# Optimization experiments

Measured on AMD Instinct MI355X. Metric: run time of the kernel, lower is better.

## Reference

```python
import jax, jax.numpy as jnp
import numpy as np

B, ENC, Hh, Ww = 32, 512, 14, 14
ATT, EMB, DEC, VOCAB = 512, 512, 512, 10000
MAXLEN = 64  # decode steps = MAXLEN - 1 = 63


def setup_inputs() -> dict:
    key = jax.random.key(0)
    ks = iter(jax.random.split(key, 40))
    def p(shape, s=0.02):
        return jax.random.normal(next(ks), shape, dtype=jnp.float32) * s
    encoder_out = jax.random.normal(next(ks), (B, ENC, Hh, Ww), dtype=jnp.float32)
    encoded_captions = jax.random.randint(next(ks), (B, MAXLEN), 0, VOCAB)
    lens = jax.random.randint(next(ks), (B,), 2, MAXLEN + 1)
    caption_lengths = jnp.sort(lens)[::-1].at[0].set(MAXLEN)  # sorted desc, max forced
    return {
        'encoder_out': encoder_out,
        'encoded_captions': encoded_captions,
        'caption_lengths': caption_lengths,
        'emb_table': p((VOCAB, EMB)),
        'W_enc_att': p((ENC, ATT)), 'b_enc_att': jnp.zeros((ATT,), jnp.float32),
        'W_dec_att': p((DEC, ATT)), 'b_dec_att': jnp.zeros((ATT,), jnp.float32),
        'W_full_att': p((ATT, 1)), 'b_full_att': jnp.zeros((1,), jnp.float32),
        'W_init_h': p((ENC, DEC)), 'b_init_h': jnp.zeros((DEC,), jnp.float32),
        'W_init_c': p((ENC, DEC)), 'b_init_c': jnp.zeros((DEC,), jnp.float32),
        'W_f_beta': p((DEC, ENC)), 'b_f_beta': jnp.zeros((ENC,), jnp.float32),
        'W_ih': p((EMB + ENC, 4 * DEC)), 'b_ih': jnp.zeros((4 * DEC,), jnp.float32),
        'W_hh': p((DEC, 4 * DEC)), 'b_hh': jnp.zeros((4 * DEC,), jnp.float32),
        'W_fc': p((DEC, VOCAB)), 'b_fc': jnp.zeros((VOCAB,), jnp.float32),
    }


def reference(encoder_out, encoded_captions, caption_lengths, emb_table,
              W_enc_att, b_enc_att, W_dec_att, b_dec_att, W_full_att, b_full_att,
              W_init_h, b_init_h, W_init_c, b_init_c, W_f_beta, b_f_beta,
              W_ih, b_ih, W_hh, b_hh, W_fc, b_fc):
    Bs, C, H, W = encoder_out.shape
    enc = encoder_out.transpose(0, 2, 3, 1).reshape(Bs, H * W, C)   # [B,P,ENC]
    emb = emb_table[encoded_captions]                               # [B,L,EMB]
    mean_enc = enc.mean(axis=1)
    h0 = mean_enc @ W_init_h + b_init_h
    c0 = mean_enc @ W_init_c + b_init_c
    dec_len = caption_lengths - 1                                   # [B]
    T = encoded_captions.shape[1] - 1                               # static 63
    enc_att = enc @ W_enc_att + b_enc_att                           # precomputed [B,P,ATT]
    emb_steps = jnp.swapaxes(emb[:, :T, :], 0, 1)                   # [T,B,EMB]
    ts = jnp.arange(T)

    def step(carry, xs):
        h, c = carry
        e_t, t = xs
        # additive attention: full_att(relu(enc_att(enc) + dec_att(h)))
        dec_a = h @ W_dec_att + b_dec_att                           # [B,ATT]
        score = (jax.nn.relu(enc_att + dec_a[:, None, :]) @ W_full_att)[..., 0] + b_full_att[0]
        alpha = jax.nn.softmax(score, axis=1)                       # [B,P]
        awe = jnp.einsum('bp,bpc->bc', alpha, enc)                  # [B,ENC]
        gate = jax.nn.sigmoid(h @ W_f_beta + b_f_beta)
        x = jnp.concatenate([e_t, gate * awe], axis=1)              # [B,EMB+ENC]
        gates = x @ W_ih + b_ih + h @ W_hh + b_hh                   # torch LSTMCell: i,f,g,o
        i, f, g, o = jnp.split(gates, 4, axis=1)
        c_new = jax.nn.sigmoid(f) * c + jax.nn.sigmoid(i) * jnp.tanh(g)
        h_new = jax.nn.sigmoid(o) * jnp.tanh(c_new)
        mask = (t < dec_len)[:, None]                               # active prefix (sorted lens)
        preds = jnp.where(mask, h_new @ W_fc + b_fc, 0.0)           # dropout in eval = identity
        h = jnp.where(mask, h_new, h)
        c = jnp.where(mask, c_new, c)
        return (h, c), preds

    (_, _), preds = jax.lax.scan(step, (h0, c0), (emb_steps, ts))
    return jnp.swapaxes(preds, 0, 1)                                # [B,T,VOCAB]
```

## Files before the change

### kernel.cpp

```cpp
#include <hip/hip_runtime.h>
#include <cstdint>
#include <cstddef>

typedef _Float16 f16;
typedef _Float16 h2 __attribute__((ext_vector_type(2)));
typedef _Float16 h8 __attribute__((ext_vector_type(8)));
typedef float f4v __attribute__((ext_vector_type(4)));

__device__ __forceinline__ h2 u2h2(unsigned u) { return __builtin_bit_cast(h2, u); }
__device__ __forceinline__ unsigned h22u(h2 v) { return __builtin_bit_cast(unsigned, v); }
__device__ __forceinline__ float2 u2f2(unsigned long long u) { return __builtin_bit_cast(float2, u); }

__device__ __forceinline__ float agent_ld_f(const float* p) {
    return __hip_atomic_load(p, __ATOMIC_RELAXED, __HIP_MEMORY_SCOPE_AGENT);
}
__device__ __forceinline__ void agent_st_f(float* p, float v) {
    __hip_atomic_store(p, v, __ATOMIC_RELAXED, __HIP_MEMORY_SCOPE_AGENT);
}
__device__ __forceinline__ void agent_add_f(float* p, float v) {
    __hip_atomic_fetch_add(p, v, __ATOMIC_RELAXED, __HIP_MEMORY_SCOPE_AGENT);
}
__device__ __forceinline__ unsigned agent_ld_u(const unsigned* p) {
    return __hip_atomic_load(p, __ATOMIC_RELAXED, __HIP_MEMORY_SCOPE_AGENT);
}
__device__ __forceinline__ void agent_st_u(unsigned* p, unsigned v) {
    __hip_atomic_store(p, v, __ATOMIC_RELAXED, __HIP_MEMORY_SCOPE_AGENT);
}
__device__ __forceinline__ unsigned long long agent_ld_u64(const unsigned long long* p) {
    return __hip_atomic_load(p, __ATOMIC_RELAXED, __HIP_MEMORY_SCOPE_AGENT);
}

__device__ __forceinline__ float fdot2(h2 a, h2 b, float c) {
#if __has_builtin(__builtin_amdgcn_fdot2)
    return __builtin_amdgcn_fdot2(a, b, c, false);
#else
    return c + (float)a.x * (float)b.x + (float)a.y * (float)b.y;
#endif
}
__device__ __forceinline__ float sigf(float x) { return 1.0f / (1.0f + expf(-x)); }

__device__ __forceinline__ void gbar32(unsigned* gflags, unsigned epoch, int local) {
    __syncthreads();
    if (threadIdx.x < 64) {
        if (threadIdx.x == 0) {
            asm volatile("s_waitcnt vmcnt(0)" ::: "memory");
            __hip_atomic_store(&gflags[local], epoch, __ATOMIC_RELAXED, __HIP_MEMORY_SCOPE_AGENT);
        }
        const int l = threadIdx.x & 31;
        bool ok;
        do {
            ok = (__hip_atomic_load(&gflags[l], __ATOMIC_RELAXED,
                                    __HIP_MEMORY_SCOPE_AGENT) >= epoch);
            if (!ok) __builtin_amdgcn_s_sleep(1);
        } while (__ballot(ok) != ~0ull);
        asm volatile("" ::: "memory");
    }
    __syncthreads();
}

__global__ void k_prep_w(const float* W_enc, const float* W_dec, const float* W_fb,
                         const float* b_dec, const float* b_fb,
                         const float* b_ih, const float* b_hh,
                         f16* W_encT, f16* Wdf8, float* b_df, float* b_cat) {
    const int S0 = 512 * 512;
    const int S2 = 512 * 1024;
    const int total = S0 + S2 + 1024 + 2048;
    for (int idx = blockIdx.x * 256 + threadIdx.x; idx < total; idx += gridDim.x * 256) {
        int i = idx;
        if (i < S0) { int n = i >> 9, k = i & 511; W_encT[i] = (f16)W_enc[k * 512 + n]; continue; }
        i -= S0;
        if (i < S2) {
            int k8 = i / 8192, r = i % 8192, col = r >> 3, kr = r & 7;
            int k = k8 * 8 + kr;
            float v = (col < 512) ? W_dec[k * 512 + col] : W_fb[k * 512 + (col - 512)];
            Wdf8[i] = (f16)v;
            continue;
        }
        i -= S2;
        if (i < 1024) { b_df[i] = (i < 512) ? b_dec[i] : b_fb[i - 512]; continue; }
        i -= 1024;
        b_cat[i] = b_ih[i] + b_hh[i];
    }
}

__global__ void k_tr_fc(const float* W_fc, f16* W_fcT) {
    __shared__ float tile[64][65];
    int n0 = blockIdx.x * 64;
    int k0 = blockIdx.y * 64;
    int t = threadIdx.x;
#pragma unroll
    for (int i = 0; i < 16; ++i) {
        int lin = t + i * 256;
        int kl = lin >> 6, nl = lin & 63;
        int n = n0 + nl;
        tile[kl][nl] = (n < 10000) ? W_fc[(long)(k0 + kl) * 10000 + n] : 0.0f;
    }
    __syncthreads();
#pragma unroll
    for (int i = 0; i < 2; ++i) {
        int lin = t + i * 256;
        int r = lin >> 3, cv = lin & 7;
        f16 v[8];
#pragma unroll
        for (int kr = 0; kr < 8; ++kr) v[kr] = (f16)tile[cv * 8 + kr][r];
        *(uint4*)&W_fcT[(long)(n0 + r) * 512 + k0 + cv * 8] = *(uint4*)v;
    }
}

__global__ void k_pack_part(const float* W_ih, const float* W_hh, f16* Wpart8) {
    __shared__ float tile[64][65];
    int k0 = blockIdx.x * 64;
    int n0 = blockIdx.y * 64;
    int t = threadIdx.x;
#pragma unroll
    for (int i = 0; i < 16; ++i) {
        int lin = t + i * 256;
        int kl = lin >> 6, nl = lin & 63;
        int k = k0 + kl;
        float v = (k < 512) ? W_ih[(long)k * 2048 + n0 + nl]
                            : W_hh[(long)(k - 512) * 2048 + n0 + nl];
        tile[kl][nl] = v;
    }
    __syncthreads();
#pragma unroll
    for (int i = 0; i < 2; ++i) {
        int lin = t + i * 256;
        int nl = lin & 63, k8l = lin >> 6;
        f16 v[8];
#pragma unroll
        for (int kr = 0; kr < 8; ++kr) v[kr] = (f16)tile[k8l * 8 + kr][nl];
        *(uint4*)&Wpart8[(long)(k0 / 8 + k8l) * 16384 + (long)(n0 + nl) * 8] = *(uint4*)v;
    }
}

__global__ void k_pack_mid(const float* W_ih, f16* Wmid8) {
    __shared__ float tile[64][65];
    int k0 = blockIdx.x * 64;
    int n0 = blockIdx.y * 64;
    int t = threadIdx.x;
#pragma unroll
    for (int i = 0; i < 16; ++i) {
        int lin = t + i * 256;
        int kl = lin >> 6, nl = lin & 63;
        tile[kl][nl] = W_ih[(long)(512 + k0 + kl) * 2048 + n0 + nl];
    }
    __syncthreads();
#pragma unroll
    for (int i = 0; i < 2; ++i) {
        int lin = t + i * 256;
        int nl = lin & 63, k8l = lin >> 6;
        f16 v[8];
#pragma unroll
        for (int kr = 0; kr < 8; ++kr) v[kr] = (f16)tile[k8l * 8 + kr][nl];
        *(uint4*)&Wmid8[(long)(k0 / 8 + k8l) * 16384 + (long)(n0 + nl) * 8] = *(uint4*)v;
    }
}

__global__ void k_prep_enc(const float* enc_out, f16* enc_t, float* mean_enc) {
    __shared__ float tile[64][197];
    int b = blockIdx.x >> 3, cc = blockIdx.x & 7, c0 = cc * 64;
    int t = threadIdx.x;
    const float* src = enc_out + ((long)b * 512 + c0) * 196;
    for (int i = 0; i < 49; ++i) {
        int lin = t + i * 256;
        int cl = lin / 196, p = lin % 196;
        tile[cl][p] = src[cl * 196 + p];
    }
    __syncthreads();
    if (t < 64) {
        float s = 0.f;
        for (int p = 0; p < 196; ++p) s += tile[t][p];
        mean_enc[b * 512 + c0 + t] = s * (1.0f / 196.0f);
    }
    __syncthreads();
    int cl = t & 63, pg = t >> 6;
    for (int i = 0; i < 49; ++i) {
        int p = pg * 49 + i;
        enc_t[((long)(b * 196 + p)) * 512 + c0 + cl] = (f16)tile[cl][p];
    }
}

__global__ void k_h0c0(const float* mean_enc, const float* W_init_h, const float* b_init_h,
                       const float* W_init_c, const float* b_init_c,
                       float* c, f16* h_h, f16* h_all, unsigned* bar) {
    if (blockIdx.x == 64) {
        int t = threadIdx.x;
        for (int i = t; i < 512; i += 256) bar[i] = 0u;
        for (int i = t; i < 32 * 512; i += 256) h_all[(long)2016 * 512 + i] = (f16)0.0f;
        return;
    }
    __shared__ float ms[512];
    int b = blockIdx.x >> 1, which = blockIdx.x & 1;
    const float* W = which ? W_init_c : W_init_h;
    const float* bb = which ? b_init_c : b_init_h;
    int t = threadIdx.x;
    ms[t] = mean_enc[b * 512 + t];
    ms[t + 256] = mean_enc[b * 512 + t + 256];
    __syncthreads();
    for (int jj = 0; jj < 2; ++jj) {
        int j = t + jj * 256;
        float acc = bb[j];
        for (int k = 0; k < 512; ++k) acc += ms[k] * W[k * 512 + j];
        if (which) c[b * 512 + j] = acc;
        else h_h[b * 512 + j] = (f16)acc;
    }
}

__global__ __launch_bounds__(256, 2) void k_encatt(const f16* A, const f16* Bt,
                                                   const float* bias, f16* Cout) {
    __shared__ __align__(16) f16 As[128 * 32];
    __shared__ __align__(16) f16 Bs[128 * 32];
    int m0 = blockIdx.x * 128, n0 = blockIdx.y * 128;
    int t = threadIdx.x, w = t >> 6, lane = t & 63;
    int wm = (w >> 1) * 64, wn = (w & 1) * 64;
    int lm = lane & 15, lq = lane >> 4;
    f4v acc[4][4];
    for (int mi = 0; mi < 4; ++mi)
        for (int ni = 0; ni < 4; ++ni) acc[mi][ni] = (f4v){0.f, 0.f, 0.f, 0.f};
    for (int kb = 0; kb < 512; kb += 32) {
        for (int i = 0; i < 2; ++i) {
            int li = t + i * 256;
            int row = li >> 2, q = li & 3;
            *(uint4*)&As[row * 32 + q * 8] = *(const uint4*)&A[(long)(m0 + row) * 512 + kb + q * 8];
            *(uint4*)&Bs[row * 32 + q * 8] = *(const uint4*)&Bt[(long)(n0 + row) * 512 + kb + q * 8];
        }
        __syncthreads();
        h8 af[4], bf[4];
        for (int i = 0; i < 4; ++i) {
            af[i] = *(const h8*)&As[(wm + i * 16 + lm) * 32 + lq * 8];
            bf[i] = *(const h8*)&Bs[(wn + i * 16 + lm) * 32 + lq * 8];
        }
        for (int mi = 0; mi < 4; ++mi)
            for (int ni = 0; ni < 4; ++ni)
                acc[mi][ni] = __builtin_amdgcn_mfma_f32_16x16x32_f16(af[mi], bf[ni], acc[mi][ni], 0, 0, 0);
        __syncthreads();
    }
    for (int mi = 0; mi < 4; ++mi)
        for (int ni = 0; ni < 4; ++ni)
            for (int r = 0; r < 4; ++r) {
                int row = m0 + wm + mi * 16 + lq * 4 + r;
                int col = n0 + wn + ni * 16 + lm;
                Cout[(long)row * 512 + col] = (f16)(acc[mi][ni][r] + bias[col]);
            }
}

__global__ __launch_bounds__(256, 2) void k_fc(const f16* A, const f16* Bt, const float* bias,
                                               const int* cl, float* out) {
    __shared__ __align__(16) f16 As[128 * 32];
    __shared__ __align__(16) f16 Bs[128 * 32];
    int m0 = blockIdx.x * 128, n0 = blockIdx.y * 128;
    int t = threadIdx.x, w = t >> 6, lane = t & 63;
    int wm = (w >> 1) * 64, wn = (w & 1) * 64;
    int lm = lane & 15, lq = lane >> 4;

    bool myact = false;
    if (t < 128) {
        int row = m0 + t;
        if (row < 2016) {
            int b = row / 63, tt = row - b * 63;
            myact = tt < (cl[b] - 1);
        }
    }
    int anyact = __syncthreads_or((int)myact);
    if (!anyact) {
        for (int i = 0; i < 64; ++i) {
            int idx = t + i * 256;
            int row = m0 + (idx >> 7), col = n0 + (idx & 127);
            if (row < 2016 && col < 10000) out[(long)row * 10000 + col] = 0.0f;
        }
        return;
    }

    f4v acc[4][4];
    for (int mi = 0; mi < 4; ++mi)
        for (int ni = 0; ni < 4; ++ni) acc[mi][ni] = (f4v){0.f, 0.f, 0.f, 0.f};
    for (int kb = 0; kb < 512; kb += 32) {
        for (int i = 0; i < 2; ++i) {
            int li = t + i * 256;
            int row = li >> 2, q = li & 3;
            *(uint4*)&As[row * 32 + q * 8] = *(const uint4*)&A[(long)(m0 + row) * 512 + kb + q * 8];
            *(uint4*)&Bs[row * 32 + q * 8] = *(const uint4*)&Bt[(long)(n0 + row) * 512 + kb + q * 8];
        }
        __syncthreads();
        h8 af[4], bf[4];
        for (int i = 0; i < 4; ++i) {
            af[i] = *(const h8*)&As[(wm + i * 16 + lm) * 32 + lq * 8];
            bf[i] = *(const h8*)&Bs[(wn + i * 16 + lm) * 32 + lq * 8];
        }
        for (int mi = 0; mi < 4; ++mi)
            for (int ni = 0; ni < 4; ++ni)
                acc[mi][ni] = __builtin_amdgcn_mfma_f32_16x16x32_f16(af[mi], bf[ni], acc[mi][ni], 0, 0, 0);
        __syncthreads();
    }
    for (int mi = 0; mi < 4; ++mi)
        for (int ni = 0; ni < 4; ++ni)
            for (int r = 0; r < 4; ++r) {
                int row = m0 + wm + mi * 16 + lq * 4 + r;
                int col = n0 + wn + ni * 16 + lm;
                if (row < 2016 && col < 10000) {
                    int b = row / 63, tt = row - b * 63;
                    bool act = tt < (cl[b] - 1);
                    out[(long)row * 10000 + col] = act ? (acc[mi][ni][r] + bias[col]) : 0.0f;
                }
            }
}

__global__ __launch_bounds__(512, 1) void k_loop(
    const f16* Wdf8, const float* b_df,
    const f16* Wpart8, const f16* Wmid8, const float* b_cat,
    const f16* enc_att_h, const f16* enc_t,
    const float* W_full, const float* emb, const int* caps, const int* cl,
    float* c, f16* h_h, float* da_gp, float* awe2, float* psum2,
    f16* h_all, unsigned* bar) {
    __shared__ __align__(16) unsigned xcat[4 * 512];
    __shared__ float gred[8 * 4 * 64];
    __shared__ float dfred[512];
    __shared__ float gp_loc[4 * 64];
    __shared__ float das2[512];
    __shared__ float es[32];
    __shared__ float ps4[4];
    __shared__ __align__(16) unsigned xms[4 * 256];
    __shared__ float g3[8 * 4 * 64];
    __shared__ float gsm[256];
    __shared__ __align__(16) f16 ea_s[25 * 512];
    __shared__ __align__(16) f16 et_s[512 * 26];

    const int bid = blockIdx.x, t = threadIdx.x;
    const int lane = t & 63, w = t >> 6;
    const int local = bid & 31;
    unsigned* gflags = bar + (bid >> 5) * 32;

    const int bg = bid >> 5, b0 = bg * 4;
    const int cg = bid & 31;
    const int jg = bid & 31;
    const int b2 = b0 + ((bid >> 3) & 3), pg = bid & 7;
    const int nr = (196 - pg * 25) < 25 ? (196 - pg * 25) : 25;

    float4 wfa = *(const float4*)(W_full + lane * 8);
    float4 wfb = *(const float4*)(W_full + lane * 8 + 4);
    const int nc3 = ((t & 63) >> 4) * 512 + jg * 16 + (t & 15);
    float bc_g = 0.f, bdf = 0.f;
    if (t < 256) bc_g = b_cat[nc3];
    if (t < 128) bdf = b_df[cg * 32 + (t & 31)];
    const int myb = b0 + (t >> 3);
    const int mycl = (t < 32) ? cl[myb] : 0;
    const int jp = t & 7;
    const int j0 = jg * 16 + jp * 2;
    const int n1 = (lane >> 4) * 512 + cg * 16 + (lane & 15);
    const int n3 = n1;
    const int dfcol = cg * 32 + (lane & 31);
    const int ksub = lane >> 5, wb2 = w & 3, kh = w >> 2;

    int steps_g;
    {
        int c0v = cl[b0], c1v = cl[b0 + 1], c2v = cl[b0 + 2], c3v = cl[b0 + 3];
        int m01 = c0v > c1v ? c0v : c1v;
        int m23 = c2v > c3v ? c2v : c3v;
        steps_g = (m01 > m23 ? m01 : m23) - 1;
    }

    {
        int r = t >> 6, cv = t & 63;
        for (int base = 0; base < 25; base += 8) {
            int rr = base + r;
            if (rr < nr) {
                const long rowoff = ((long)b2 * 196 + pg * 25 + rr) * 512 + cv * 8;
                uint4 va = *(const uint4*)(enc_att_h + rowoff);
                *(uint4*)&ea_s[rr * 512 + cv * 8] = va;
                uint4 vt = *(const uint4*)(enc_t + rowoff);
                f16 tmp[8]; *(uint4*)tmp = vt;
#pragma unroll
                for (int e = 0; e < 8; ++e) et_s[(cv * 8 + e) * 26 + rr] = tmp[e];
            }
        }
    }

    for (int step = 0; step < steps_g; ++step) {
        {
            if (t < 64) {
                int idx = local * 64 + t;
                agent_st_f(awe2 + (long)(b0 + (idx >> 9)) * 512 + (idx & 511), 0.f);
            }
            if (local == 0 && t < 4) agent_st_f(psum2 + b0 + t, 0.f);
#pragma unroll
            for (int i = 0; i < 2; ++i) {
                int idx = t + i * 512;
                int b = idx >> 8, off = idx & 255;
                int tok = caps[(b0 + b) * 64 + step];
                float2 ev = *(const float2*)(emb + (long)tok * 512 + off * 2);
                h2 pe; pe.x = (f16)ev.x; pe.y = (f16)ev.y;
                xcat[b * 512 + off] = h22u(pe);
                xcat[b * 512 + 256 + off] = agent_ld_u((const unsigned*)h_h + (b0 + b) * 256 + off);
            }
            __syncthreads();
            {
                const f16* wp = Wpart8 + (long)n1 * 8;
                float a0 = 0.f, a1 = 0.f, a2 = 0.f, a3 = 0.f;
                for (int kk = 0; kk < 16; ++kk) {
                    int k8 = w * 16 + kk;
                    uint4 wv = *(const uint4*)(wp + (long)k8 * 16384);
                    uint4 x0 = *(const uint4*)&xcat[0 * 512 + k8 * 4];
                    uint4 x1 = *(const uint4*)&xcat[1 * 512 + k8 * 4];
                    uint4 x2 = *(const uint4*)&xcat[2 * 512 + k8 * 4];
                    uint4 x3 = *(const uint4*)&xcat[3 * 512 + k8 * 4];
                    a0 = fdot2(u2h2(x0.x), u2h2(wv.x), a0);
                    a0 = fdot2(u2h2(x0.y), u2h2(wv.y), a0);
                    a0 = fdot2(u2h2(x0.z), u2h2(wv.z), a0);
                    a0 = fdot2(u2h2(x0.w), u2h2(wv.w), a0);
                    a1 = fdot2(u2h2(x1.x), u2h2(wv.x), a1);
                    a1 = fdot2(u2h2(x1.y), u2h2(wv.y), a1);
                    a1 = fdot2(u2h2(x1.z), u2h2(wv.z), a1);
                    a1 = fdot2(u2h2(x1.w), u2h2(wv.w), a1);
                    a2 = fdot2(u2h2(x2.x), u2h2(wv.x), a2);
                    a2 = fdot2(u2h2(x2.y), u2h2(wv.y), a2);
                    a2 = fdot2(u2h2(x2.z), u2h2(wv.z), a2);
                    a2 = fdot2(u2h2(x2.w), u2h2(wv.w), a2);
                    a3 = fdot2(u2h2(x3.x), u2h2(wv.x), a3);
                    a3 = fdot2(u2h2(x3.y), u2h2(wv.y), a3);
                    a3 = fdot2(u2h2(x3.z), u2h2(wv.z), a3);
                    a3 = fdot2(u2h2(x3.w), u2h2(wv.w), a3);
                }
                gred[(w * 4 + 0) * 64 + lane] = a0;
                gred[(w * 4 + 1) * 64 + lane] = a1;
                gred[(w * 4 + 2) * 64 + lane] = a2;
                gred[(w * 4 + 3) * 64 + lane] = a3;
            }
            {
                const f16* wdf = Wdf8 + (long)dfcol * 8;
                const unsigned* hx = &xcat[wb2 * 512 + 256];
                int kbase = kh * 32 + ksub * 16;
                float a = 0.f;
                for (int kk = 0; kk < 16; ++kk) {
                    int k8 = kbase + kk;
                    uint4 wv = *(const uint4*)(wdf + (long)k8 * 8192);
                    uint4 xv = *(const uint4*)&hx[k8 * 4];
                    a = fdot2(u2h2(xv.x), u2h2(wv.x), a);
                    a = fdot2(u2h2(xv.y), u2h2(wv.y), a);
                    a = fdot2(u2h2(xv.z), u2h2(wv.z), a);
                    a = fdot2(u2h2(xv.w), u2h2(wv.w), a);
                }
                dfred[(wb2 * 32 + (lane & 31)) * 4 + kh * 2 + ksub] = a;
            }
            __syncthreads();
            if (t < 256) {
                int b = t >> 6, col = t & 63;
                float v = bc_g;
#pragma unroll
                for (int ww = 0; ww < 8; ++ww) v += gred[(ww * 4 + b) * 64 + col];
                gp_loc[b * 64 + col] = v;
            }
            if (t < 128) {
                int b = t >> 5, col = t & 31;
                const float* dr = &dfred[(b * 32 + col) * 4];
                float v = dr[0] + dr[1] + dr[2] + dr[3] + bdf;
                agent_st_f(da_gp + (long)(b0 + b) * 1024 + cg * 32 + col, v);
            }
        }
        gbar32(gflags, (unsigned)step * 3u + 1u, local);

        {
            das2[t] = agent_ld_f(da_gp + (long)b2 * 1024 + t);
            __syncthreads();
            float4 dv0 = *(const float4*)&das2[lane * 8];
            float4 dv1 = *(const float4*)&das2[lane * 8 + 4];
#pragma unroll
            for (int i = 0; i < 4; ++i) {
                int r = w + i * 8;
                if (r < nr) {
                    uint4 ev = *(const uint4*)&ea_s[r * 512 + lane * 8];
                    h2 e0 = u2h2(ev.x), e1 = u2h2(ev.y), e2 = u2h2(ev.z), e3 = u2h2(ev.w);
                    float a = 0.f;
                    a += fmaxf((float)e0.x + dv0.x, 0.f) * wfa.x;
                    a += fmaxf((float)e0.y + dv0.y, 0.f) * wfa.y;
                    a += fmaxf((float)e1.x + dv0.z, 0.f) * wfa.z;
                    a += fmaxf((float)e1.y + dv0.w, 0.f) * wfa.w;
                    a += fmaxf((float)e2.x + dv1.x, 0.f) * wfb.x;
                    a += fmaxf((float)e2.y + dv1.y, 0.f) * wfb.y;
                    a += fmaxf((float)e3.x + dv1.z, 0.f) * wfb.z;
                    a += fmaxf((float)e3.y + dv1.w, 0.f) * wfb.w;
                    for (int m = 32; m; m >>= 1) a += __shfl_xor(a, m);
                    if (lane == 0) es[r] = expf(a);
                }
            }
            __syncthreads();
            {
                float acc = 0.f;
                for (int r = 0; r < nr; ++r) acc += es[r] * (float)et_s[t * 26 + r];
                agent_add_f(awe2 + (long)b2 * 512 + t, acc);
                if (t == 0) {
                    float s = 0.f;
                    for (int r = 0; r < nr; ++r) s += es[r];
                    agent_add_f(psum2 + b2, s);
                }
            }
        }
        gbar32(gflags, (unsigned)step * 3u + 2u, local);

        {
            if (t < 4) ps4[t] = 1.0f / agent_ld_f(psum2 + b0 + t);
            __syncthreads();
#pragma unroll
            for (int i = 0; i < 2; ++i) {
                int idx = t + i * 512;
                int bb = idx >> 8, cp = idx & 255;
                float2 aw = u2f2(agent_ld_u64(
                    (const unsigned long long*)awe2 + (long)(b0 + bb) * 256 + cp));
                float inv = ps4[bb];
                float2 fb = u2f2(agent_ld_u64(
                    (const unsigned long long*)da_gp + (long)(b0 + bb) * 512 + 256 + cp));
                h2 pa;
                pa.x = (f16)(sigf(fb.x) * aw.x * inv);
                pa.y = (f16)(sigf(fb.y) * aw.y * inv);
                xms[bb * 256 + cp] = h22u(pa);
            }
            __syncthreads();
            {
                const f16* wp = Wmid8 + (long)n3 * 8;
                float a0 = 0.f, a1 = 0.f, a2 = 0.f, a3 = 0.f;
                for (int kk = 0; kk < 8; ++kk) {
                    int k8 = w * 8 + kk;
                    uint4 wv = *(const uint4*)(wp + (long)k8 * 16384);
                    uint4 x0 = *(const uint4*)&xms[0 * 256 + k8 * 4];
                    uint4 x1 = *(const uint4*)&xms[1 * 256 + k8 * 4];
                    uint4 x2 = *(const uint4*)&xms[2 * 256 + k8 * 4];
                    uint4 x3 = *(const uint4*)&xms[3 * 256 + k8 * 4];
                    a0 = fdot2(u2h2(x0.x), u2h2(wv.x), a0);
                    a0 = fdot2(u2h2(x0.y), u2h2(wv.y), a0);
                    a0 = fdot2(u2h2(x0.z), u2h2(wv.z), a0);
                    a0 = fdot2(u2h2(x0.w), u2h2(wv.w), a0);
                    a1 = fdot2(u2h2(x1.x), u2h2(wv.x), a1);
                    a1 = fdot2(u2h2(x1.y), u2h2(wv.y), a1);
                    a1 = fdot2(u2h2(x1.z), u2h2(wv.z), a1);
                    a1 = fdot2(u2h2(x1.w), u2h2(wv.w), a1);
                    a2 = fdot2(u2h2(x2.x), u2h2(wv.x), a2);
                    a2 = fdot2(u2h2(x2.y), u2h2(wv.y), a2);
                    a2 = fdot2(u2h2(x2.z), u2h2(wv.z), a2);
                    a2 = fdot2(u2h2(x2.w), u2h2(wv.w), a2);
                    a3 = fdot2(u2h2(x3.x), u2h2(wv.x), a3);
                    a3 = fdot2(u2h2(x3.y), u2h2(wv.y), a3);
                    a3 = fdot2(u2h2(x3.z), u2h2(wv.z), a3);
                    a3 = fdot2(u2h2(x3.w), u2h2(wv.w), a3);
                }
                g3[(w * 4 + 0) * 64 + lane] = a0;
                g3[(w * 4 + 1) * 64 + lane] = a1;
                g3[(w * 4 + 2) * 64 + lane] = a2;
                g3[(w * 4 + 3) * 64 + lane] = a3;
            }
            __syncthreads();
            if (t < 256) {
                int b = t >> 6, l2 = t & 63;
                float v = gp_loc[b * 64 + l2];
#pragma unroll
                for (int ww = 0; ww < 8; ++ww) v += g3[(ww * 4 + b) * 64 + l2];
                gsm[b * 64 + l2] = v;
            }
            __syncthreads();
            if (t < 32) {
                int bl = t >> 3;
                int l0 = jp * 2, l1 = jp * 2 + 1;
                float gi0 = gsm[bl * 64 + l0],      gi1 = gsm[bl * 64 + l1];
                float gf0 = gsm[bl * 64 + 16 + l0], gf1 = gsm[bl * 64 + 16 + l1];
                float gg0 = gsm[bl * 64 + 32 + l0], gg1 = gsm[bl * 64 + 32 + l1];
                float go0 = gsm[bl * 64 + 48 + l0], go1 = gsm[bl * 64 + 48 + l1];
                float2 cold = *(float2*)(c + (long)myb * 512 + j0);
                float cn0 = sigf(gf0) * cold.x + sigf(gi0) * tanhf(gg0);
                float hn0 = sigf(go0) * tanhf(cn0);
                float cn1 = sigf(gf1) * cold.y + sigf(gi1) * tanhf(gg1);
                float hn1 = sigf(go1) * tanhf(cn1);
                h2 oldh = u2h2(agent_ld_u((const unsigned*)h_h + myb * 256 + (j0 >> 1)));
                bool act = step < (mycl - 1);
                float hv0, hv1, cv0, cv1;
                if (act) { hv0 = hn0; hv1 = hn1; cv0 = cn0; cv1 = cn1; }
                else { hv0 = (float)oldh.x; hv1 = (float)oldh.y; cv0 = cold.x; cv1 = cold.y; }
                float2 cw; cw.x = cv0; cw.y = cv1;
                *(float2*)(c + (long)myb * 512 + j0) = cw;
                h2 hp; hp.x = (f16)hv0; hp.y = (f16)hv1;
                unsigned pv = h22u(hp);
                agent_st_u((unsigned*)h_h + myb * 256 + (j0 >> 1), pv);
                *((unsigned*)h_all + ((long)myb * 63 + step) * 256 + (j0 >> 1)) = pv;
            }
        }
        gbar32(gflags, (unsigned)step * 3u + 3u, local);
    }
}

extern "C" void kernel_launch(void* const* d_in, const int* in_sizes, int n_in,
                              void* d_out, int out_size, void* d_ws, size_t ws_size,
                              hipStream_t stream) {
    const float* encoder_out = (const float*)d_in[0];
    const int* caps = (const int*)d_in[1];
    const int* cl = (const int*)d_in[2];
    const float* emb = (const float*)d_in[3];
    const float* W_enc_att = (const float*)d_in[4];
    const float* b_enc_att = (const float*)d_in[5];
    const float* W_dec_att = (const float*)d_in[6];
    const float* b_dec_att = (const float*)d_in[7];
    const float* W_full_att = (const float*)d_in[8];
    const float* W_init_h = (const float*)d_in[10];
    const float* b_init_h = (const float*)d_in[11];
    const float* W_init_c = (const float*)d_in[12];
    const float* b_init_c = (const float*)d_in[13];
    const float* W_f_beta = (const float*)d_in[14];
    const float* b_f_beta = (const float*)d_in[15];
    const float* W_ih = (const float*)d_in[16];
    const float* b_ih = (const float*)d_in[17];
    const float* W_hh = (const float*)d_in[18];
    const float* b_hh = (const float*)d_in[19];
    const float* W_fc = (const float*)d_in[20];
    const float* b_fc = (const float*)d_in[21];

    char* p = (char*)d_ws;
    auto take = [&](size_t bytes) {
        char* r = p;
        p += (bytes + 255) & ~(size_t)255;
        return r;
    };
    f16* enc_t     = (f16*)take((size_t)32 * 196 * 512 * 2);
    f16* enc_att_h = (f16*)take((size_t)32 * 196 * 512 * 2);
    f16* W_encT    = (f16*)take((size_t)512 * 512 * 2);
    f16* W_fcT     = (f16*)take((size_t)10112 * 512 * 2);
    f16* Wdf8      = (f16*)take((size_t)512 * 1024 * 2);
    f16* Wpart8    = (f16*)take((size_t)1024 * 2048 * 2);
    f16* Wmid8     = (f16*)take((size_t)512 * 2048 * 2);
    f16* h_all     = (f16*)take((size_t)2048 * 512 * 2);
    f16* h_h       = (f16*)take((size_t)32 * 512 * 2);
    float* b_df    = (float*)take(1024 * 4);
    float* b_cat   = (float*)take(2048 * 4);
    float* mean_e  = (float*)take((size_t)32 * 512 * 4);
    float* c_st    = (float*)take((size_t)32 * 512 * 4);
    float* da_gp   = (float*)take((size_t)32 * 1024 * 4);
    float* awe2    = (float*)take((size_t)32 * 512 * 4);
    float* psum2   = (float*)take((size_t)32 * 4);
    unsigned* bar  = (unsigned*)take(2048);

    k_prep_w<<<1024, 256, 0, stream>>>(W_enc_att, W_dec_att, W_f_beta,
                                       b_dec_att, b_f_beta, b_ih, b_hh,
                                       W_encT, Wdf8, b_df, b_cat);
    k_tr_fc<<<dim3(158, 8), 256, 0, stream>>>(W_fc, W_fcT);
    k_pack_part<<<dim3(16, 32), 256, 0, stream>>>(W_ih, W_hh, Wpart8);
    k_pack_mid<<<dim3(8, 32), 256, 0, stream>>>(W_ih, Wmid8);
    k_prep_enc<<<256, 256, 0, stream>>>(encoder_out, enc_t, mean_e);
    k_h0c0<<<65, 256, 0, stream>>>(mean_e, W_init_h, b_init_h, W_init_c, b_init_c,
                                   c_st, h_h, h_all, bar);
    k_encatt<<<dim3(49, 4), 256, 0, stream>>>(enc_t, W_encT, b_enc_att, enc_att_h);
    k_loop<<<256, 512, 0, stream>>>(Wdf8, b_df, Wpart8, Wmid8, b_cat,
                                    enc_att_h, enc_t, W_full_att, emb, caps, cl,
                                    c_st, h_h, da_gp, awe2, psum2, h_all, bar);
    k_fc<<<dim3(16, 79), 256, 0, stream>>>(h_all, W_fcT, b_fc, cl, (float*)d_out);
}
```

Measured before the change: 1.616 ms.

## Cache Wmid weight slice in LDS and prefetch next-step embeddings

Each block now loads its slice of the Wmid weight matrix into a new 64 KB shared-memory buffer once, before the time loop. The per-step mid GEMV then reads weights from LDS instead of global memory or L2. The embedding lookup for step+1 is moved to just after the mid-stage barrier, so it leaves the start of the next step. This raises LDS use per block close to the CU limit, which could limit occupancy or fail to launch if the budget is exceeded.

New measurement: 1.564 ms. -3.2%, faster.

```diff
diff --git a/kernel.cpp b/kernel.cpp
--- a/kernel.cpp
+++ b/kernel.cpp
@@ -324,6 +324,7 @@
     __shared__ float gsm[256];
     __shared__ __align__(16) f16 ea_s[25 * 512];
     __shared__ __align__(16) f16 et_s[512 * 26];
+    __shared__ __align__(16) f16 mid_s[64 * 512];
 
     const int bid = blockIdx.x, t = threadIdx.x;
     const int lane = t & 63, w = t >> 6;
@@ -347,9 +348,9 @@
     const int jp = t & 7;
     const int j0 = jg * 16 + jp * 2;
     const int n1 = (lane >> 4) * 512 + cg * 16 + (lane & 15);
-    const int n3 = n1;
     const int dfcol = cg * 32 + (lane & 31);
     const int ksub = lane >> 5, wb2 = w & 3, kh = w >> 2;
+    const int ci_l = (lane >> 4) * 16 + (lane & 15);
 
     int steps_g;
     {
@@ -373,6 +374,23 @@
                 for (int e = 0; e < 8; ++e) et_s[(cv * 8 + e) * 26 + rr] = tmp[e];
             }
         }
+#pragma unroll
+        for (int i = 0; i < 8; ++i) {
+            int u = t + i * 512;
+            int k8 = u >> 6, ci = u & 63;
+            int n = (ci >> 4) * 512 + jg * 16 + (ci & 15);
+            *(uint4*)&mid_s[k8 * 512 + ci * 8] =
+                *(const uint4*)(Wmid8 + (long)k8 * 16384 + (long)n * 8);
+        }
+#pragma unroll
+        for (int i = 0; i < 2; ++i) {
+            int idx = t + i * 512;
+            int b = idx >> 8, off = idx & 255;
+            int tok = caps[(b0 + b) * 64 + 0];
+            float2 ev = *(const float2*)(emb + (long)tok * 512 + off * 2);
+            h2 pe; pe.x = (f16)ev.x; pe.y = (f16)ev.y;
+            xcat[b * 512 + off] = h22u(pe);
+        }
     }
 
     for (int step = 0; step < steps_g; ++step) {
@@ -386,10 +404,6 @@
             for (int i = 0; i < 2; ++i) {
                 int idx = t + i * 512;
                 int b = idx >> 8, off = idx & 255;
-                int tok = caps[(b0 + b) * 64 + step];
-                float2 ev = *(const float2*)(emb + (long)tok * 512 + off * 2);
-                h2 pe; pe.x = (f16)ev.x; pe.y = (f16)ev.y;
-                xcat[b * 512 + off] = h22u(pe);
                 xcat[b * 512 + 256 + off] = agent_ld_u((const unsigned*)h_h + (b0 + b) * 256 + off);
             }
             __syncthreads();
@@ -515,11 +529,22 @@
             }
             __syncthreads();
             {
-                const f16* wp = Wmid8 + (long)n3 * 8;
+#pragma unroll
+                for (int i = 0; i < 2; ++i) {
+                    int idx = t + i * 512;
+                    int b = idx >> 8, off = idx & 255;
+                    int tok = caps[(b0 + b) * 64 + step + 1];
+                    float2 ev = *(const float2*)(emb + (long)tok * 512 + off * 2);
+                    h2 pe; pe.x = (f16)ev.x; pe.y = (f16)ev.y;
+                    xcat[b * 512 + off] = h22u(pe);
+                }
+            }
+            {
+                const f16* wp = mid_s + ci_l * 8;
                 float a0 = 0.f, a1 = 0.f, a2 = 0.f, a3 = 0.f;
                 for (int kk = 0; kk < 8; ++kk) {
                     int k8 = w * 8 + kk;
-                    uint4 wv = *(const uint4*)(wp + (long)k8 * 16384);
+                    uint4 wv = *(const uint4*)(wp + k8 * 512);
                     uint4 x0 = *(const uint4*)&xms[0 * 256 + k8 * 4];
                     uint4 x1 = *(const uint4*)&xms[1 * 256 + k8 * 4];
                     uint4 x2 = *(const uint4*)&xms[2 * 256 + k8 * 4];
```
